# Performance work log

Measured on AMD Instinct MI355X. Metric: run time of the kernel, lower is better.

The kernel has to match this reference:

```python
import jax, jax.numpy as jnp
import numpy as np

N_HEAD = 8


def setup_inputs() -> dict:
    key = jax.random.key(0)
    ks = jax.random.split(key, 12)
    b, l, d_q, d_o, h, w = 32, 64, 1024, 512, 32, 32

    def rn(k, shape, s=0.02):
        return jax.random.normal(k, shape, jnp.float32) * s

    return {
        "q": jax.random.normal(ks[0], (b, l, d_q), jnp.float32),
        "v": jax.random.normal(ks[1], (b, d_o, h, w), jnp.float32),
        "mask": jax.random.bernoulli(ks[2], 0.2, (b, l)),
        "w_qs_w": rn(ks[3], (d_o, d_q)), "w_qs_b": jnp.zeros((d_o,), jnp.float32),
        "w_qs_att_w": rn(ks[4], (1, d_o)), "w_qs_att_b": jnp.zeros((1,), jnp.float32),
        "w_kc_w": rn(ks[5], (d_o, d_o, 1, 1)), "w_kc_b": jnp.zeros((d_o,), jnp.float32),
        "w_kd_w": rn(ks[6], (d_o, d_o, 1, 1)), "w_kd_b": jnp.zeros((d_o,), jnp.float32),
        "w_vs_w": rn(ks[7], (d_o, d_o, 1, 1)), "w_vs_b": jnp.zeros((d_o,), jnp.float32),
        "w_m_w": rn(ks[8], (1, d_o, 3, 3)), "w_m_b": jnp.zeros((1,), jnp.float32),
        "bn_gamma": jnp.ones((d_o,), jnp.float32), "bn_beta": jnp.zeros((d_o,), jnp.float32),
        "bn_mean": jnp.zeros((d_o,), jnp.float32), "bn_var": jnp.ones((d_o,), jnp.float32),
    }


def _conv1x1(x, wgt, bias):  # x: (b,c,h,w), wgt: (o,c,1,1)
    return jnp.einsum('bchw,oc->bohw', x, wgt[:, :, 0, 0]) + bias[None, :, None, None]


def reference(q, v, mask, w_qs_w, w_qs_b, w_qs_att_w, w_qs_att_b,
              w_kc_w, w_kc_b, w_kd_w, w_kd_b, w_vs_w, w_vs_b,
              w_m_w, w_m_b, bn_gamma, bn_beta, bn_mean, bn_var):
    b, l, _ = q.shape
    _, c, h, w_ = v.shape
    n = N_HEAD
    dk = c // n
    temp = float(np.power(dk, 0.5))  # sqrt(d_o // n_head)
    residual = v

    qp = q @ w_qs_w.T + w_qs_b                       # (b,l,d_o)
    flap = qp @ w_qs_att_w.T + w_qs_att_b            # (b,l,1)
    flap = jnp.where(mask[:, :, None], -1e9, flap)
    flap = jax.nn.softmax(flap, axis=-1)             # softmax over size-1 dim -> all ones (faithful to torch)

    kc = _conv1x1(v, w_kc_w, w_kc_b).reshape(b, n, dk, h * w_).transpose(0, 1, 3, 2)  # (b,n,hw,dk)
    kd = _conv1x1(v, w_kd_w, w_kd_b).reshape(b, n, dk, h * w_).transpose(0, 1, 3, 2)
    vh = _conv1x1(v, w_vs_w, w_vs_b).reshape(b, n, dk, h * w_).transpose(0, 1, 3, 2)
    qh = qp.reshape(b, l, n, dk).transpose(0, 2, 1, 3)                                 # (b,n,l,dk)

    # Collect: bmm -> weight by flap -> reduce over l -> softmax over hw -> bmm with v
    attn_col = jnp.einsum('bnld,bnsd->bnls', qh, kc)                 # (b,n,l,hw)
    attn_col = (attn_col * flap[:, None, :, :]).sum(axis=2, keepdims=True) / temp  # (b,n,1,hw)
    attn_col = jax.nn.softmax(attn_col, axis=-1)
    attn = jnp.einsum('bnus,bnsd->bnud', attn_col, vh)               # (b,n,1,dk)

    # Diffuse: bmm -> weight by flap^T -> reduce over l -> sigmoid -> outer product
    attn_dif = jnp.einsum('bnsd,bnld->bnsl', kd, qh)                 # (b,n,hw,l)
    flap_t = flap.transpose(0, 2, 1)[:, None]                        # (b,1,1,l)
    attn_dif = jax.nn.sigmoid((attn_dif * flap_t).sum(-1, keepdims=True) / temp)  # (b,n,hw,1)
    output = attn_dif * attn                                         # (b,n,hw,dk)

    # Faithful to torch permute(0,1,4,3,2).view(b,-1,h,w) (requires h==w)
    out = output.reshape(b, n, h, w_, dk).transpose(0, 1, 4, 3, 2).reshape(b, c, h, w_)
    attn_map = out

    m = jax.lax.conv_general_dilated(out, w_m_w, (1, 1), 'SAME',
                                     dimension_numbers=('NCHW', 'OIHW', 'NCHW'))
    m_attn = (m + w_m_b[None, :, None, None]).reshape(b, h * w_)

    eps = 1e-5  # BatchNorm2d eval mode
    scale = bn_gamma / jnp.sqrt(bn_var + eps)
    out = (out - bn_mean[None, :, None, None]) * scale[None, :, None, None] + bn_beta[None, :, None, None]
    out = out + residual
    out = jnp.where(out >= 0, out, 0.1 * out)  # LeakyReLU(0.1)
    return (out, m_attn, attn_map)
```

## Files before the change

kernel.cpp:

```cpp
#include <hip/hip_runtime.h>


#define BB 32
#define LL 64
#define DQn 1024
#define CCn 512
#define NH 8
#define DKn 64
#define HWn 1024

__global__ void k1_qsum_pre(const float* __restrict__ q, float* __restrict__ qsp) {
    int b = blockIdx.y;
    int dq = blockIdx.x * 256 + threadIdx.x;
    const float* qp = q + (size_t)b * LL * DQn + dq;
    float acc = 0.f;
#pragma unroll 8
    for (int l = 0; l < LL; ++l) acc += qp[l * DQn];
    qsp[b * DQn + dq] = acc;
}

__global__ void k2_qsum(const float* __restrict__ qsp, const float* __restrict__ w,
                        const float* __restrict__ bias, float* __restrict__ qs) {
    int dof = blockIdx.x;
    int t = threadIdx.x;
    int b = t & 31, ch = t >> 5;
    const float* wrow = w + (size_t)dof * DQn + ch * 128;
    const float* qrow = qsp + (size_t)b * DQn + ch * 128;
    float acc = 0.f;
#pragma unroll 8
    for (int i = 0; i < 128; i += 4) {
        float4 wv = *reinterpret_cast<const float4*>(wrow + i);
        float4 qv = *reinterpret_cast<const float4*>(qrow + i);
        acc += wv.x * qv.x + wv.y * qv.y + wv.z * qv.z + wv.w * qv.w;
    }
    __shared__ float scr[256];
    scr[t] = acc;
    __syncthreads();
    if (t < 32) {
        float a = 0.f;
#pragma unroll
        for (int c2 = 0; c2 < 8; ++c2) a += scr[c2 * 32 + t];
        qs[t * CCn + dof] = a + 64.f * bias[dof];
    }
}

__global__ void k3_wq(const float* __restrict__ qs,
                      const float* __restrict__ wkc, const float* __restrict__ bkc,
                      const float* __restrict__ wkd, const float* __restrict__ bkd,
                      float* __restrict__ wq, float* __restrict__ bq) {
    int cc = blockIdx.x, wsel = blockIdx.y, b = blockIdx.z;
    const float* w = wsel ? wkd : wkc;
    int cl = threadIdx.x & 31, n = threadIdx.x >> 5;
    int c = cc * 32 + cl;
    const float* qrow = qs + b * CCn + n * DKn;
    const float* wrow = w + (size_t)(n * DKn) * CCn + c;
    float acc = 0.f;
#pragma unroll 8
    for (int d = 0; d < DKn; ++d)
        acc += qrow[d] * wrow[(size_t)d * CCn];
    wq[((size_t)b * CCn + c) * 16 + wsel * 8 + n] = acc;
    if (cc == 0 && b == 0) {
        const float* bw = wsel ? bkd : bkc;
        int pp = threadIdx.x, bb = pp >> 3, nn = pp & 7;
        float a2 = 0.f;
#pragma unroll 8
        for (int d = 0; d < DKn; ++d)
            a2 += qs[bb * CCn + nn * DKn + d] * bw[nn * DKn + d];
        bq[wsel * 256 + pp] = a2;
    }
}

__global__ void __launch_bounds__(256) k4_score(
        const float* __restrict__ v, const float* __restrict__ wq,
        const float* __restrict__ bq, float* __restrict__ score,
        float* __restrict__ dsig) {
    int sc = blockIdx.x, b = blockIdx.y;
    int sl = threadIdx.x & 63;
    int g = threadIdx.x >> 6;
    __shared__ float red[4][64][17];
    float ak[16];
#pragma unroll
    for (int j = 0; j < 16; ++j) ak[j] = 0.f;
    int s = sc * 64 + sl;
    const float* vp = v + ((size_t)(b * CCn + g * 128)) * HWn + s;
    const float* wqb = wq + ((size_t)b * CCn + g * 128) * 16;
#pragma unroll 4
    for (int c = 0; c < 128; ++c) {
        float vv = vp[(size_t)c * HWn];
        const float* wc = wqb + c * 16;
#pragma unroll
        for (int j = 0; j < 16; ++j) ak[j] += wc[j] * vv;
    }
#pragma unroll
    for (int j = 0; j < 16; ++j) red[g][sl][j] = ak[j];
    __syncthreads();
    int t = threadIdx.x;
    if (t < 64) {
#pragma unroll
        for (int n = 0; n < 8; ++n) {
            float skc = red[0][t][n] + red[1][t][n] + red[2][t][n] + red[3][t][n];
            float skd = red[0][t][8 + n] + red[1][t][8 + n] + red[2][t][8 + n] + red[3][t][8 + n];
            skc = (skc + bq[b * 8 + n]) * 0.125f;
            skd = (skd + bq[256 + b * 8 + n]) * 0.125f;
            int ss = sc * 64 + t;
            score[(b * NH + n) * HWn + ss] = skc;
            dsig[(b * NH + n) * HWn + ss] = 1.f / (1.f + __expf(-skd));
        }
    }
}

__global__ void k5_softmax(const float* __restrict__ score, float* __restrict__ pt) {
    int n = blockIdx.x, b = blockIdx.y;
    const float* srow = score + (b * NH + n) * HWn;
    int t = threadIdx.x;
    float4 sv = *reinterpret_cast<const float4*>(srow + 4 * t);
    float m = fmaxf(fmaxf(sv.x, sv.y), fmaxf(sv.z, sv.w));
#pragma unroll
    for (int off = 32; off > 0; off >>= 1) m = fmaxf(m, __shfl_xor(m, off));
    __shared__ float red[4];
    __shared__ float red2[4];
    int w = t >> 6, lane = t & 63;
    if (lane == 0) red[w] = m;
    __syncthreads();
    m = fmaxf(fmaxf(red[0], red[1]), fmaxf(red[2], red[3]));
    float e0 = __expf(sv.x - m), e1 = __expf(sv.y - m);
    float e2 = __expf(sv.z - m), e3 = __expf(sv.w - m);
    float ssum = e0 + e1 + e2 + e3;
#pragma unroll
    for (int off = 32; off > 0; off >>= 1) ssum += __shfl_xor(ssum, off);
    if (lane == 0) red2[w] = ssum;
    __syncthreads();
    ssum = red2[0] + red2[1] + red2[2] + red2[3];
    float inv = 1.f / ssum;
    float* pb = pt + ((size_t)b * HWn + 4 * t) * 8 + n;
    pb[0] = e0 * inv;
    pb[8] = e1 * inv;
    pb[16] = e2 * inv;
    pb[24] = e3 * inv;
}

__global__ void __launch_bounds__(256) k6_pvp(
        const float* __restrict__ v, const float* __restrict__ pt,
        float* __restrict__ pvp) {
    int cc = blockIdx.x, sc = blockIdx.y, b = blockIdx.z;
    int c = cc * 256 + threadIdx.x;
    const float* vp = v + ((size_t)b * CCn + c) * HWn + sc * 128;
    const float* pb = pt + ((size_t)b * HWn + sc * 128) * 8;
    float acc[NH];
#pragma unroll
    for (int n = 0; n < NH; ++n) acc[n] = 0.f;
#pragma unroll 2
    for (int s4 = 0; s4 < 32; ++s4) {
        float4 v4 = *reinterpret_cast<const float4*>(vp + 4 * s4);
        const float* pp = pb + s4 * 32;
#pragma unroll
        for (int n = 0; n < NH; ++n)
            acc[n] += pp[n] * v4.x + pp[8 + n] * v4.y + pp[16 + n] * v4.z + pp[24 + n] * v4.w;
    }
#pragma unroll
    for (int n = 0; n < NH; ++n)
        pvp[((sc * BB + b) * NH + n) * CCn + c] = acc[n];
}

__global__ void k7_attn(const float* __restrict__ pvp, const float* __restrict__ wvs,
                        const float* __restrict__ bvs, float* __restrict__ attn) {
    int n = blockIdx.x, b = blockIdx.y;
    __shared__ float pvl[CCn];
    __shared__ float scr[64 * 5];
    int t = threadIdx.x;
    for (int c = t; c < CCn; c += 256) {
        float acc = 0.f;
#pragma unroll
        for (int sc = 0; sc < 8; ++sc)
            acc += pvp[((sc * BB + b) * NH + n) * CCn + c];
        pvl[c] = acc;
    }
    __syncthreads();
    int d = t & 63, qq = t >> 6;
    const float* wrow = wvs + (size_t)(n * DKn + d) * CCn + qq * 128;
    const float* pq = pvl + qq * 128;
    float acc = 0.f;
#pragma unroll 4
    for (int i = 0; i < 128; ++i) acc += pq[i] * wrow[i];
    scr[d * 5 + qq] = acc;
    __syncthreads();
    if (t < 64) {
        float a = scr[t * 5] + scr[t * 5 + 1] + scr[t * 5 + 2] + scr[t * 5 + 3]
                + bvs[n * DKn + t];
        attn[(b * NH + n) * DKn + t] = a;
    }
}

__global__ void k8_mattn(const float* __restrict__ dsig, const float* __restrict__ attn,
                         const float* __restrict__ wm, const float* __restrict__ wmb,
                         float* __restrict__ out1) {
    int b = blockIdx.x;
    __shared__ float dst[NH * 1056];
    __shared__ float al[CCn];
    __shared__ float A2[NH * 9];
    int t = threadIdx.x;
    al[t] = attn[b * CCn + t];
    al[t + 256] = attn[b * CCn + t + 256];
    for (int g = t; g < NH * HWn; g += 256) {
        int n = g >> 10, s = g & 1023;
        dst[n * 1056 + (s & 31) * 33 + (s >> 5)] = dsig[b * NH * HWn + g];
    }
    __syncthreads();
    if (t < 72) {
        int n = t / 9, tap = t % 9;
        float acc = 0.f;
#pragma unroll 8
        for (int d = 0; d < DKn; ++d)
            acc += al[n * DKn + d] * wm[(n * DKn + d) * 9 + tap];
        A2[t] = acc;
    }
    __syncthreads();
    float bm = wmb[0];
    for (int pos = t; pos < HWn; pos += 256) {
        int y = pos >> 5, x = pos & 31;
        float m = 0.f;
#pragma unroll
        for (int n = 0; n < NH; ++n) {
            const float* dn = dst + n * 1056;
#pragma unroll
            for (int dy = 0; dy < 3; ++dy) {
                int yy = y + dy - 1;
                if ((unsigned)yy < 32u) {
#pragma unroll
                    for (int dx = 0; dx < 3; ++dx) {
                        int xx = x + dx - 1;
                        if ((unsigned)xx < 32u)
                            m += A2[n * 9 + dy * 3 + dx] * dn[yy * 33 + xx];
                    }
                }
            }
        }
        out1[b * HWn + pos] = m + bm;
    }
}

__global__ void __launch_bounds__(256) k9_out(
        const float* __restrict__ v, const float* __restrict__ dsig,
        const float* __restrict__ attn,
        const float* __restrict__ gamma, const float* __restrict__ beta,
        const float* __restrict__ mean, const float* __restrict__ var,
        float* __restrict__ out0, float* __restrict__ out2) {
    int dh = blockIdx.x, n = blockIdx.y, b = blockIdx.z;
    __shared__ float dst[1056];
    __shared__ float al[16], bnA[16], bnB[16];
    int t = threadIdx.x;
#pragma unroll
    for (int k = 0; k < 4; ++k) {
        int s = t + k * 256;
        dst[(s & 31) * 33 + (s >> 5)] = dsig[(b * NH + n) * HWn + s];
    }
    if (t < 16) {
        int d = dh * 16 + t;
        al[t] = attn[(b * NH + n) * DKn + d];
        int ch = n * DKn + d;
        float A = gamma[ch] * rsqrtf(var[ch] + 1e-5f);
        bnA[t] = A;
        bnB[t] = beta[ch] - mean[ch] * A;
    }
    __syncthreads();
    int y = t >> 3, x = (t & 7) * 4;
    const float* dr = dst + y * 33 + x;
#pragma unroll 2
    for (int k = 0; k < 16; ++k) {
        int d = dh * 16 + k;
        size_t base = (((size_t)(b * CCn + n * DKn + d)) << 10) + y * 32 + x;
        float4 v4 = *reinterpret_cast<const float4*>(v + base);
        float a = al[k], A = bnA[k], Bc = bnB[k];
        float p0 = a * dr[0], p1 = a * dr[1], p2 = a * dr[2], p3 = a * dr[3];
        float4 mo = make_float4(p0, p1, p2, p3);
        *reinterpret_cast<float4*>(out2 + base) = mo;
        float o0 = p0 * A + Bc + v4.x;
        float o1 = p1 * A + Bc + v4.y;
        float o2 = p2 * A + Bc + v4.z;
        float o3 = p3 * A + Bc + v4.w;
        o0 = o0 < 0.f ? 0.1f * o0 : o0;
        o1 = o1 < 0.f ? 0.1f * o1 : o1;
        o2 = o2 < 0.f ? 0.1f * o2 : o2;
        o3 = o3 < 0.f ? 0.1f * o3 : o3;
        float4 oo = make_float4(o0, o1, o2, o3);
        *reinterpret_cast<float4*>(out0 + base) = oo;
    }
}

extern "C" void kernel_launch(void* const* d_in, const int* in_sizes, int n_in,
                              void* d_out, int out_size, void* d_ws, size_t ws_size,
                              hipStream_t stream) {
    (void)in_sizes; (void)n_in; (void)out_size; (void)ws_size;
    const float* q   = (const float*)d_in[0];
    const float* v   = (const float*)d_in[1];
    const float* wqs = (const float*)d_in[3];
    const float* bqs = (const float*)d_in[4];
    const float* wkc = (const float*)d_in[7];
    const float* bkc = (const float*)d_in[8];
    const float* wkd = (const float*)d_in[9];
    const float* bkd = (const float*)d_in[10];
    const float* wvs = (const float*)d_in[11];
    const float* bvs = (const float*)d_in[12];
    const float* wm  = (const float*)d_in[13];
    const float* wmb = (const float*)d_in[14];
    const float* gam = (const float*)d_in[15];
    const float* bet = (const float*)d_in[16];
    const float* mea = (const float*)d_in[17];
    const float* var = (const float*)d_in[18];

    float* ws = (float*)d_ws;
    float* dsig  = ws + 0;
    float* pt    = ws + 262144;
    float* pvp   = ws + 524288;
    float* score = ws + 524288;
    float* wq    = ws + 786432;
    float* qsp   = ws + 1048576;
    float* qs    = ws + 1081344;
    float* bq    = ws + 1097728;
    float* attn  = ws + 1572864;

    float* out0 = (float*)d_out;
    float* out1 = out0 + 16777216;
    float* out2 = out1 + 32768;

    k1_qsum_pre<<<dim3(4, 32), 256, 0, stream>>>(q, qsp);
    k2_qsum<<<dim3(512), 256, 0, stream>>>(qsp, wqs, bqs, qs);
    k3_wq<<<dim3(16, 2, 32), 256, 0, stream>>>(qs, wkc, bkc, wkd, bkd, wq, bq);
    k4_score<<<dim3(16, 32), 256, 0, stream>>>(v, wq, bq, score, dsig);
    k5_softmax<<<dim3(8, 32), 256, 0, stream>>>(score, pt);
    k6_pvp<<<dim3(2, 8, 32), 256, 0, stream>>>(v, pt, pvp);
    k7_attn<<<dim3(8, 32), 256, 0, stream>>>(pvp, wvs, bvs, attn);
    k8_mattn<<<dim3(32), 256, 0, stream>>>(dsig, attn, wm, wmb, out1);
    k9_out<<<dim3(4, 8, 32), 256, 0, stream>>>(v, dsig, attn, gam, bet, mea, var, out0, out2);
}
```

Measured before the change: 370.8 us.

## Fuse score, softmax and P·V into one kernel with bf16 LDS tile

Measured after the change: 347.2 us. -6.4%, faster.

```diff
diff --git a/kernel.cpp b/kernel.cpp
--- a/kernel.cpp
+++ b/kernel.cpp
@@ -8,6 +8,18 @@
 #define NH 8
 #define DKn 64
 #define HWn 1024
+
+typedef unsigned short u16;
+typedef unsigned int u32;
+
+__device__ __forceinline__ float bfr(u16 u) {
+    return __uint_as_float(((u32)u) << 16);
+}
+__device__ __forceinline__ u16 f2bf(float f) {
+    u32 x = __float_as_uint(f);
+    u32 r = (x + 0x7FFFu + ((x >> 16) & 1u)) >> 16;
+    return (u16)r;
+}
 
 __global__ void k1_qsum_pre(const float* __restrict__ q, float* __restrict__ qsp) {
     int b = blockIdx.y;
@@ -70,109 +82,110 @@
     }
 }
 
-__global__ void __launch_bounds__(256) k4_score(
+__global__ void __launch_bounds__(256) k46_scorepv(
         const float* __restrict__ v, const float* __restrict__ wq,
-        const float* __restrict__ bq, float* __restrict__ score,
-        float* __restrict__ dsig) {
+        const float* __restrict__ bq, float* __restrict__ dsig,
+        float* __restrict__ pvp, float* __restrict__ sums) {
     int sc = blockIdx.x, b = blockIdx.y;
-    int sl = threadIdx.x & 63;
-    int g = threadIdx.x >> 6;
-    __shared__ float red[4][64][17];
-    float ak[16];
-#pragma unroll
-    for (int j = 0; j < 16; ++j) ak[j] = 0.f;
-    int s = sc * 64 + sl;
-    const float* vp = v + ((size_t)(b * CCn + g * 128)) * HWn + s;
-    const float* wqb = wq + ((size_t)b * CCn + g * 128) * 16;
+    __shared__ u16 vt[CCn * 33];
+    __shared__ float red[4][32][17];
+    __shared__ float et[32 * 8];
+    int t = threadIdx.x;
+    int s0 = sc * 32;
+
+    {
+        int s = t & 31, c2 = t >> 5;
+        const float* vb = v + ((size_t)(b * CCn + c2 * 64) << 10) + s0 + s;
+#pragma unroll 8
+        for (int cr = 0; cr < 64; ++cr)
+            vt[(c2 * 64 + cr) * 33 + s] = f2bf(vb[(size_t)cr << 10]);
+    }
+    __syncthreads();
+
+    {
+        int s = t & 31, g = t >> 5;
+        float ak[16];
+#pragma unroll
+        for (int j = 0; j < 16; ++j) ak[j] = 0.f;
+        const float* wqb = wq + ((size_t)b * CCn + g * 64) * 16;
 #pragma unroll 4
-    for (int c = 0; c < 128; ++c) {
-        float vv = vp[(size_t)c * HWn];
-        const float* wc = wqb + c * 16;
-#pragma unroll
-        for (int j = 0; j < 16; ++j) ak[j] += wc[j] * vv;
-    }
-#pragma unroll
-    for (int j = 0; j < 16; ++j) red[g][sl][j] = ak[j];
-    __syncthreads();
-    int t = threadIdx.x;
-    if (t < 64) {
-#pragma unroll
-        for (int n = 0; n < 8; ++n) {
-            float skc = red[0][t][n] + red[1][t][n] + red[2][t][n] + red[3][t][n];
-            float skd = red[0][t][8 + n] + red[1][t][8 + n] + red[2][t][8 + n] + red[3][t][8 + n];
-            skc = (skc + bq[b * 8 + n]) * 0.125f;
-            skd = (skd + bq[256 + b * 8 + n]) * 0.125f;
-            int ss = sc * 64 + t;
-            score[(b * NH + n) * HWn + ss] = skc;
-            dsig[(b * NH + n) * HWn + ss] = 1.f / (1.f + __expf(-skd));
-        }
-    }
-}
-
-__global__ void k5_softmax(const float* __restrict__ score, float* __restrict__ pt) {
-    int n = blockIdx.x, b = blockIdx.y;
-    const float* srow = score + (b * NH + n) * HWn;
-    int t = threadIdx.x;
-    float4 sv = *reinterpret_cast<const float4*>(srow + 4 * t);
-    float m = fmaxf(fmaxf(sv.x, sv.y), fmaxf(sv.z, sv.w));
-#pragma unroll
-    for (int off = 32; off > 0; off >>= 1) m = fmaxf(m, __shfl_xor(m, off));
-    __shared__ float red[4];
-    __shared__ float red2[4];
-    int w = t >> 6, lane = t & 63;
-    if (lane == 0) red[w] = m;
-    __syncthreads();
-    m = fmaxf(fmaxf(red[0], red[1]), fmaxf(red[2], red[3]));
-    float e0 = __expf(sv.x - m), e1 = __expf(sv.y - m);
-    float e2 = __expf(sv.z - m), e3 = __expf(sv.w - m);
-    float ssum = e0 + e1 + e2 + e3;
-#pragma unroll
-    for (int off = 32; off > 0; off >>= 1) ssum += __shfl_xor(ssum, off);
-    if (lane == 0) red2[w] = ssum;
-    __syncthreads();
-    ssum = red2[0] + red2[1] + red2[2] + red2[3];
-    float inv = 1.f / ssum;
-    float* pb = pt + ((size_t)b * HWn + 4 * t) * 8 + n;
-    pb[0] = e0 * inv;
-    pb[8] = e1 * inv;
-    pb[16] = e2 * inv;
-    pb[24] = e3 * inv;
-}
-
-__global__ void __launch_bounds__(256) k6_pvp(
-        const float* __restrict__ v, const float* __restrict__ pt,
-        float* __restrict__ pvp) {
-    int cc = blockIdx.x, sc = blockIdx.y, b = blockIdx.z;
-    int c = cc * 256 + threadIdx.x;
-    const float* vp = v + ((size_t)b * CCn + c) * HWn + sc * 128;
-    const float* pb = pt + ((size_t)b * HWn + sc * 128) * 8;
-    float acc[NH];
-#pragma unroll
-    for (int n = 0; n < NH; ++n) acc[n] = 0.f;
+        for (int i = 0; i < 64; ++i) {
+            float vv = bfr(vt[(g * 64 + i) * 33 + s]);
+            const float* wc = wqb + i * 16;
+#pragma unroll
+            for (int j = 0; j < 16; ++j) ak[j] += wc[j] * vv;
+        }
+#pragma unroll
+        for (int j = 0; j < 16; ++j) ak[j] += __shfl_xor(ak[j], 32);
+        int wv = t >> 6;
+        if ((t & 63) < 32) {
+#pragma unroll
+            for (int j = 0; j < 16; ++j) red[wv][s][j] = ak[j];
+        }
+    }
+    __syncthreads();
+    if (t < 32) {
+        int s = t;
+#pragma unroll
+        for (int n = 0; n < NH; ++n) {
+            float rc = red[0][s][n] + red[1][s][n] + red[2][s][n] + red[3][s][n];
+            float rd = red[0][s][8 + n] + red[1][s][8 + n] + red[2][s][8 + n] + red[3][s][8 + n];
+            float skc = (rc + bq[b * 8 + n]) * 0.125f;
+            float skd = (rd + bq[256 + b * 8 + n]) * 0.125f;
+            et[s * 8 + n] = __expf(skc);
+            dsig[(b * NH + n) * HWn + s0 + s] = 1.f / (1.f + __expf(-skd));
+        }
+    }
+    __syncthreads();
+    if (t < 8) {
+        float a = 0.f;
+#pragma unroll
+        for (int s = 0; s < 32; ++s) a += et[s * 8 + t];
+        sums[(b * NH + t) * 32 + sc] = a;
+    }
+    {
+        float acc0[NH], acc1[NH];
+#pragma unroll
+        for (int n = 0; n < NH; ++n) { acc0[n] = 0.f; acc1[n] = 0.f; }
 #pragma unroll 2
-    for (int s4 = 0; s4 < 32; ++s4) {
-        float4 v4 = *reinterpret_cast<const float4*>(vp + 4 * s4);
-        const float* pp = pb + s4 * 32;
-#pragma unroll
-        for (int n = 0; n < NH; ++n)
-            acc[n] += pp[n] * v4.x + pp[8 + n] * v4.y + pp[16 + n] * v4.z + pp[24 + n] * v4.w;
-    }
-#pragma unroll
-    for (int n = 0; n < NH; ++n)
-        pvp[((sc * BB + b) * NH + n) * CCn + c] = acc[n];
-}
-
-__global__ void k7_attn(const float* __restrict__ pvp, const float* __restrict__ wvs,
-                        const float* __restrict__ bvs, float* __restrict__ attn) {
+        for (int s = 0; s < 32; ++s) {
+            float4 ea = *reinterpret_cast<const float4*>(et + s * 8);
+            float4 eb = *reinterpret_cast<const float4*>(et + s * 8 + 4);
+            float va = bfr(vt[t * 33 + s]);
+            float vb2 = bfr(vt[(t + 256) * 33 + s]);
+            acc0[0] += ea.x * va; acc0[1] += ea.y * va; acc0[2] += ea.z * va; acc0[3] += ea.w * va;
+            acc0[4] += eb.x * va; acc0[5] += eb.y * va; acc0[6] += eb.z * va; acc0[7] += eb.w * va;
+            acc1[0] += ea.x * vb2; acc1[1] += ea.y * vb2; acc1[2] += ea.z * vb2; acc1[3] += ea.w * vb2;
+            acc1[4] += eb.x * vb2; acc1[5] += eb.y * vb2; acc1[6] += eb.z * vb2; acc1[7] += eb.w * vb2;
+        }
+        size_t base = ((size_t)sc * BB + b) * NH;
+#pragma unroll
+        for (int n = 0; n < NH; ++n) {
+            pvp[(base + n) * CCn + t] = acc0[n];
+            pvp[(base + n) * CCn + t + 256] = acc1[n];
+        }
+    }
+}
+
+__global__ void k7_attn(const float* __restrict__ pvp, const float* __restrict__ sums,
+                        const float* __restrict__ wvs, const float* __restrict__ bvs,
+                        float* __restrict__ attn) {
     int n = blockIdx.x, b = blockIdx.y;
     __shared__ float pvl[CCn];
     __shared__ float scr[64 * 5];
-    int t = threadIdx.x;
+    __shared__ float sinv;
+    int t = threadIdx.x;
+    if (t == 0) {
+        float a = 0.f;
+#pragma unroll
+        for (int sc = 0; sc < 32; ++sc) a += sums[(b * NH + n) * 32 + sc];
+        sinv = 1.f / a;
+    }
     for (int c = t; c < CCn; c += 256) {
         float acc = 0.f;
-#pragma unroll
-        for (int sc = 0; sc < 8; ++sc)
-            acc += pvp[((sc * BB + b) * NH + n) * CCn + c];
+#pragma unroll 4
+        for (int sc = 0; sc < 32; ++sc)
+            acc += pvp[(((size_t)sc * BB + b) * NH + n) * CCn + c];
         pvl[c] = acc;
     }
     __syncthreads();
@@ -185,7 +198,7 @@
     scr[d * 5 + qq] = acc;
     __syncthreads();
     if (t < 64) {
-        float a = scr[t * 5] + scr[t * 5 + 1] + scr[t * 5 + 2] + scr[t * 5 + 3]
+        float a = (scr[t * 5] + scr[t * 5 + 1] + scr[t * 5 + 2] + scr[t * 5 + 3]) * sinv
                 + bvs[n * DKn + t];
         attn[(b * NH + n) * DKn + t] = a;
     }
@@ -309,15 +322,14 @@
     const float* var = (const float*)d_in[18];
 
     float* ws = (float*)d_ws;
-    float* dsig  = ws + 0;
-    float* pt    = ws + 262144;
-    float* pvp   = ws + 524288;
-    float* score = ws + 524288;
-    float* wq    = ws + 786432;
-    float* qsp   = ws + 1048576;
-    float* qs    = ws + 1081344;
-    float* bq    = ws + 1097728;
-    float* attn  = ws + 1572864;
+    float* qsp  = ws + 0;
+    float* qs   = ws + 32768;
+    float* wq   = ws + 49152;
+    float* bq   = ws + 311296;
+    float* dsig = ws + 311808;
+    float* sums = ws + 573952;
+    float* attn = ws + 582144;
+    float* pvp  = ws + 598528;
 
     float* out0 = (float*)d_out;
     float* out1 = out0 + 16777216;
@@ -326,10 +338,8 @@
     k1_qsum_pre<<<dim3(4, 32), 256, 0, stream>>>(q, qsp);
     k2_qsum<<<dim3(512), 256, 0, stream>>>(qsp, wqs, bqs, qs);
     k3_wq<<<dim3(16, 2, 32), 256, 0, stream>>>(qs, wkc, bkc, wkd, bkd, wq, bq);
-    k4_score<<<dim3(16, 32), 256, 0, stream>>>(v, wq, bq, score, dsig);
-    k5_softmax<<<dim3(8, 32), 256, 0, stream>>>(score, pt);
-    k6_pvp<<<dim3(2, 8, 32), 256, 0, stream>>>(v, pt, pvp);
-    k7_attn<<<dim3(8, 32), 256, 0, stream>>>(pvp, wvs, bvs, attn);
+    k46_scorepv<<<dim3(32, 32), 256, 0, stream>>>(v, wq, bq, dsig, pvp, sums);
+    k7_attn<<<dim3(8, 32), 256, 0, stream>>>(pvp, sums, wvs, bvs, attn);
     k8_mattn<<<dim3(32), 256, 0, stream>>>(dsig, attn, wm, wmb, out1);
     k9_out<<<dim3(4, 8, 32), 256, 0, stream>>>(v, dsig, attn, gam, bet, mea, var, out0, out2);
 }
```
